# Kernel optimization log

Hardware: AMD Instinct MI355X
Metric: run time of the kernel (lower is better)

Reference implementation:

```python
import jax, jax.numpy as jnp
import numpy as np

IN_FEATURES = 8192
OUT_FEATURES = 8192
BATCH = 256


def setup_inputs() -> dict:
    key = jax.random.key(0)
    k_x, k_w, k_s, k_b = jax.random.split(key, 4)
    x = jax.random.normal(k_x, (BATCH, IN_FEATURES), dtype=jnp.float32)
    int8_weights = jax.random.randint(k_w, (OUT_FEATURES, IN_FEATURES), -128, 128, dtype=jnp.int8)
    int8_scales = jax.random.normal(k_s, (1,), dtype=jnp.float32)
    bias = jax.random.normal(k_b, (1, OUT_FEATURES), dtype=jnp.float32)
    return {"x": x, "int8_weights": int8_weights, "int8_scales": int8_scales, "bias": bias}


def reference(x, int8_weights, int8_scales, bias):
    # dequantize: symmetric per-tensor scale, then cast to activation dtype
    weights = int8_weights.astype(x.dtype) * int8_scales.astype(x.dtype)  # [out, in]
    # F.linear: x @ W^T
    out = jnp.einsum('bi,oi->bo', x, weights)
    out = out + bias
    return out
```

## Files before the change

### kernel.cpp

```cpp
#include <hip/hip_runtime.h>

#define M_DIM 256
#define N_DIM 8192
#define K_DIM 8192
#define BN 128
#define BK 32
#define KSPLIT 4
#define KLEN (K_DIM / KSPLIT)
#define NT (KLEN / BK)

typedef _Float16 half_t;
typedef __attribute__((ext_vector_type(8))) _Float16 half8;
typedef __attribute__((ext_vector_type(4))) float f32x4;
typedef __attribute__((ext_vector_type(4))) unsigned int u32x4;

__device__ __forceinline__ unsigned int pk2(float a, float b) {
  return __builtin_bit_cast(unsigned int, __builtin_amdgcn_cvt_pkrtz(a, b));
}

__global__ __launch_bounds__(512, 2) void qgemm(
    const float* __restrict__ x, const int* __restrict__ Wq,
    const float* __restrict__ scales, const float* __restrict__ bias,
    float* __restrict__ out) {
  __shared__ __align__(1024) char lds[49152];

  const int tid = threadIdx.x;
  const int bid = blockIdx.x;
  const int p = bid & 7;
  const int g = bid >> 3;
  const int ks = p >> 1;
  const int t = (g << 1) | (p & 1);
  const int col0 = t * BN;
  const int kbase = ks * KLEN;

  const int wid = tid >> 6, lane = tid & 63;
  const int wm = wid >> 1, wn = wid & 1;
  const int r16 = lane & 15, g4 = lane >> 4;

  const int xr = tid >> 1, xh2 = tid & 1;
  const int wr = tid >> 2, wc = tid & 3;

  const float* xp = x + (size_t)xr * K_DIM + kbase + xh2 * 16;
  const int* wp = Wq + (size_t)(col0 + wr) * K_DIM + kbase + wc * 8;

  const int sA = (xr >> 1) & 3;
  const int aw0 = xr * 64 + (((xh2 * 2 + 0) ^ sA) << 4);
  const int aw1 = xr * 64 + (((xh2 * 2 + 1) ^ sA) << 4);
  const int sB = (wr >> 1) & 3;
  const int bw0 = 16384 + wr * 64 + ((wc ^ sB) << 4);

  int aoff[4], boff[4];
#pragma unroll
  for (int mf = 0; mf < 4; ++mf) {
    int ra = wm * 64 + mf * 16 + r16;
    aoff[mf] = ra * 64 + ((g4 ^ ((ra >> 1) & 3)) << 4);
  }
#pragma unroll
  for (int nf = 0; nf < 4; ++nf) {
    int rb = wn * 64 + nf * 16 + r16;
    boff[nf] = 16384 + rb * 64 + ((g4 ^ ((rb >> 1) & 3)) << 4);
  }

  f32x4 acc[4][4];
#pragma unroll
  for (int i = 0; i < 4; ++i)
#pragma unroll
    for (int j = 0; j < 4; ++j) acc[i][j] = (f32x4){0.f, 0.f, 0.f, 0.f};

  float4 X0 = *(const float4*)(xp);
  float4 X1 = *(const float4*)(xp + 4);
  float4 X2 = *(const float4*)(xp + 8);
  float4 X3 = *(const float4*)(xp + 12);
  int4 Wa = *(const int4*)(wp);
  int4 Wb = *(const int4*)(wp + 4);

  for (int kt = 0; kt < NT; ++kt) {
    char* B0 = lds + (kt & 1) * 24576;

    u32x4 pa0, pa1, pb;
    pa0.x = pk2(X0.x, X0.y); pa0.y = pk2(X0.z, X0.w);
    pa0.z = pk2(X1.x, X1.y); pa0.w = pk2(X1.z, X1.w);
    pa1.x = pk2(X2.x, X2.y); pa1.y = pk2(X2.z, X2.w);
    pa1.z = pk2(X3.x, X3.y); pa1.w = pk2(X3.z, X3.w);
    pb.x = pk2((float)Wa.x, (float)Wa.y); pb.y = pk2((float)Wa.z, (float)Wa.w);
    pb.z = pk2((float)Wb.x, (float)Wb.y); pb.w = pk2((float)Wb.z, (float)Wb.w);
    *(u32x4*)(B0 + aw0) = pa0;
    *(u32x4*)(B0 + aw1) = pa1;
    *(u32x4*)(B0 + bw0) = pb;

    if (kt + 1 < NT) {
      xp += BK; wp += BK;
      X0 = *(const float4*)(xp);
      X1 = *(const float4*)(xp + 4);
      X2 = *(const float4*)(xp + 8);
      X3 = *(const float4*)(xp + 12);
      Wa = *(const int4*)(wp);
      Wb = *(const int4*)(wp + 4);
    }

    asm volatile("s_waitcnt lgkmcnt(0)" ::: "memory");
    __builtin_amdgcn_s_barrier();
    __builtin_amdgcn_sched_barrier(0);

    half8 af[4], bf[4];
#pragma unroll
    for (int mf = 0; mf < 4; ++mf) af[mf] = *(const half8*)(B0 + aoff[mf]);
#pragma unroll
    for (int nf = 0; nf < 4; ++nf) bf[nf] = *(const half8*)(B0 + boff[nf]);
#pragma unroll
    for (int mf = 0; mf < 4; ++mf)
#pragma unroll
      for (int nf = 0; nf < 4; ++nf)
        acc[mf][nf] = __builtin_amdgcn_mfma_f32_16x16x32_f16(
            af[mf], bf[nf], acc[mf][nf], 0, 0, 0);
  }

  const float scale = scales[0];
#pragma unroll
  for (int nf = 0; nf < 4; ++nf) {
    const int gcol = col0 + wn * 64 + nf * 16 + r16;
    const float bv = (ks == 0) ? bias[gcol] : 0.0f;
#pragma unroll
    for (int mf = 0; mf < 4; ++mf) {
      const int grow0 = wm * 64 + mf * 16 + g4 * 4;
#pragma unroll
      for (int j = 0; j < 4; ++j) {
        atomicAdd(out + (size_t)(grow0 + j) * N_DIM + gcol,
                  scale * acc[mf][nf][j] + bv);
      }
    }
  }
}

extern "C" void kernel_launch(void* const* d_in, const int* in_sizes, int n_in,
                              void* d_out, int out_size, void* d_ws, size_t ws_size,
                              hipStream_t stream) {
  const float* x = (const float*)d_in[0];
  const int* Wq = (const int*)d_in[1];
  const float* scales = (const float*)d_in[2];
  const float* bias = (const float*)d_in[3];
  float* out = (float*)d_out;

  hipMemsetAsync(d_out, 0, (size_t)M_DIM * N_DIM * sizeof(float), stream);
  qgemm<<<dim3(256), dim3(512), 0, stream>>>(x, Wq, scales, bias, out);
}
```

Baseline: 424.2 us.

## Pre-convert activations to fp16 tiles and stream them via direct global-to-LDS loads

```diff
diff --git a/kernel.cpp b/kernel.cpp
--- a/kernel.cpp
+++ b/kernel.cpp
@@ -8,6 +8,9 @@
 #define KSPLIT 4
 #define KLEN (K_DIM / KSPLIT)
 #define NT (KLEN / BK)
+#define ABYTES 16384
+#define BBYTES 8192
+#define BUFB (ABYTES + BBYTES)
 
 typedef _Float16 half_t;
 typedef __attribute__((ext_vector_type(8))) _Float16 half8;
@@ -17,12 +20,31 @@
 __device__ __forceinline__ unsigned int pk2(float a, float b) {
   return __builtin_bit_cast(unsigned int, __builtin_amdgcn_cvt_pkrtz(a, b));
 }
+__device__ __forceinline__ void gl16(const void* g, void* l) {
+  __builtin_amdgcn_global_load_lds(
+      (const __attribute__((address_space(1))) unsigned int*)g,
+      (__attribute__((address_space(3))) unsigned int*)l, 16, 0, 0);
+}
+
+__global__ __launch_bounds__(256) void convert_x(const float* __restrict__ x,
+                                                 half_t* __restrict__ xh) {
+  const int gid = blockIdx.x * 256 + threadIdx.x;
+  const int row = gid >> 10;
+  const int k0 = (gid & 1023) << 3;
+  float4 v0 = *(const float4*)(x + (size_t)row * K_DIM + k0);
+  float4 v1 = *(const float4*)(x + (size_t)row * K_DIM + k0 + 4);
+  half8 h;
+  h[0] = (half_t)v0.x; h[1] = (half_t)v0.y; h[2] = (half_t)v0.z; h[3] = (half_t)v0.w;
+  h[4] = (half_t)v1.x; h[5] = (half_t)v1.y; h[6] = (half_t)v1.z; h[7] = (half_t)v1.w;
+  const int kt = k0 >> 5, kk = k0 & 31;
+  *(half8*)(xh + (size_t)kt * 8192 + row * 32 + kk) = h;
+}
 
 __global__ __launch_bounds__(512, 2) void qgemm(
-    const float* __restrict__ x, const int* __restrict__ Wq,
+    const half_t* __restrict__ xh, const int* __restrict__ Wq,
     const float* __restrict__ scales, const float* __restrict__ bias,
     float* __restrict__ out) {
-  __shared__ __align__(1024) char lds[49152];
+  __shared__ __align__(1024) char lds[2 * BUFB];
 
   const int tid = threadIdx.x;
   const int bid = blockIdx.x;
@@ -31,35 +53,21 @@
   const int ks = p >> 1;
   const int t = (g << 1) | (p & 1);
   const int col0 = t * BN;
-  const int kbase = ks * KLEN;
 
   const int wid = tid >> 6, lane = tid & 63;
   const int wm = wid >> 1, wn = wid & 1;
   const int r16 = lane & 15, g4 = lane >> 4;
 
-  const int xr = tid >> 1, xh2 = tid & 1;
+  const half_t* abase = xh + (size_t)(ks * NT) * 8192;
   const int wr = tid >> 2, wc = tid & 3;
-
-  const float* xp = x + (size_t)xr * K_DIM + kbase + xh2 * 16;
-  const int* wp = Wq + (size_t)(col0 + wr) * K_DIM + kbase + wc * 8;
-
-  const int sA = (xr >> 1) & 3;
-  const int aw0 = xr * 64 + (((xh2 * 2 + 0) ^ sA) << 4);
-  const int aw1 = xr * 64 + (((xh2 * 2 + 1) ^ sA) << 4);
-  const int sB = (wr >> 1) & 3;
-  const int bw0 = 16384 + wr * 64 + ((wc ^ sB) << 4);
+  const int* wp0 = Wq + (size_t)(col0 + wr) * K_DIM + ks * KLEN + wc * 8;
+  const int wlds = ABYTES + wr * 64 + wc * 16;
 
   int aoff[4], boff[4];
 #pragma unroll
-  for (int mf = 0; mf < 4; ++mf) {
-    int ra = wm * 64 + mf * 16 + r16;
-    aoff[mf] = ra * 64 + ((g4 ^ ((ra >> 1) & 3)) << 4);
-  }
+  for (int mf = 0; mf < 4; ++mf) aoff[mf] = (wm * 64 + mf * 16 + r16) * 64 + g4 * 16;
 #pragma unroll
-  for (int nf = 0; nf < 4; ++nf) {
-    int rb = wn * 64 + nf * 16 + r16;
-    boff[nf] = 16384 + rb * 64 + ((g4 ^ ((rb >> 1) & 3)) << 4);
-  }
+  for (int nf = 0; nf < 4; ++nf) boff[nf] = ABYTES + (wn * 64 + nf * 16 + r16) * 64 + g4 * 16;
 
   f32x4 acc[4][4];
 #pragma unroll
@@ -67,52 +75,58 @@
 #pragma unroll
     for (int j = 0; j < 4; ++j) acc[i][j] = (f32x4){0.f, 0.f, 0.f, 0.f};
 
-  float4 X0 = *(const float4*)(xp);
-  float4 X1 = *(const float4*)(xp + 4);
-  float4 X2 = *(const float4*)(xp + 8);
-  float4 X3 = *(const float4*)(xp + 12);
-  int4 Wa = *(const int4*)(wp);
-  int4 Wb = *(const int4*)(wp + 4);
+  int4 Wa, Wb;
+  {
+    int4 w0a = *(const int4*)(wp0);
+    int4 w0b = *(const int4*)(wp0 + 4);
+    gl16(abase + tid * 8, lds + tid * 16);
+    gl16(abase + 4096 + tid * 8, lds + 8192 + tid * 16);
+    __builtin_amdgcn_sched_barrier(0);
+    u32x4 pb;
+    pb.x = pk2((float)w0a.x, (float)w0a.y); pb.y = pk2((float)w0a.z, (float)w0a.w);
+    pb.z = pk2((float)w0b.x, (float)w0b.y); pb.w = pk2((float)w0b.z, (float)w0b.w);
+    *(u32x4*)(lds + wlds) = pb;
+    Wa = *(const int4*)(wp0 + 32);
+    Wb = *(const int4*)(wp0 + 36);
+    __builtin_amdgcn_sched_barrier(0);
+    asm volatile("s_waitcnt vmcnt(2) lgkmcnt(0)" ::: "memory");
+    __builtin_amdgcn_s_barrier();
+  }
 
   for (int kt = 0; kt < NT; ++kt) {
-    char* B0 = lds + (kt & 1) * 24576;
+    char* Bc = lds + (kt & 1) * BUFB;
+    char* Bn = lds + ((kt & 1) ^ 1) * BUFB;
 
-    u32x4 pa0, pa1, pb;
-    pa0.x = pk2(X0.x, X0.y); pa0.y = pk2(X0.z, X0.w);
-    pa0.z = pk2(X1.x, X1.y); pa0.w = pk2(X1.z, X1.w);
-    pa1.x = pk2(X2.x, X2.y); pa1.y = pk2(X2.z, X2.w);
-    pa1.z = pk2(X3.x, X3.y); pa1.w = pk2(X3.z, X3.w);
+    u32x4 pb;
     pb.x = pk2((float)Wa.x, (float)Wa.y); pb.y = pk2((float)Wa.z, (float)Wa.w);
     pb.z = pk2((float)Wb.x, (float)Wb.y); pb.w = pk2((float)Wb.z, (float)Wb.w);
-    *(u32x4*)(B0 + aw0) = pa0;
-    *(u32x4*)(B0 + aw1) = pa1;
-    *(u32x4*)(B0 + bw0) = pb;
+    *(u32x4*)(Bn + wlds) = pb;
 
-    if (kt + 1 < NT) {
-      xp += BK; wp += BK;
-      X0 = *(const float4*)(xp);
-      X1 = *(const float4*)(xp + 4);
-      X2 = *(const float4*)(xp + 8);
-      X3 = *(const float4*)(xp + 12);
-      Wa = *(const int4*)(wp);
-      Wb = *(const int4*)(wp + 4);
-    }
+    const int an = (kt + 1 < NT) ? kt + 1 : NT - 1;
+    const half_t* asrc = abase + (size_t)an * 8192;
+    gl16(asrc + tid * 8, Bn + tid * 16);
+    gl16(asrc + 4096 + tid * 8, Bn + 8192 + tid * 16);
+    __builtin_amdgcn_sched_barrier(0);
 
-    asm volatile("s_waitcnt lgkmcnt(0)" ::: "memory");
-    __builtin_amdgcn_s_barrier();
-    __builtin_amdgcn_sched_barrier(0);
+    const int w2 = (kt + 2 < NT) ? kt + 2 : NT - 1;
+    Wa = *(const int4*)(wp0 + (size_t)w2 * 32);
+    Wb = *(const int4*)(wp0 + (size_t)w2 * 32 + 4);
 
     half8 af[4], bf[4];
 #pragma unroll
-    for (int mf = 0; mf < 4; ++mf) af[mf] = *(const half8*)(B0 + aoff[mf]);
+    for (int mf = 0; mf < 4; ++mf) af[mf] = *(const half8*)(Bc + aoff[mf]);
 #pragma unroll
-    for (int nf = 0; nf < 4; ++nf) bf[nf] = *(const half8*)(B0 + boff[nf]);
+    for (int nf = 0; nf < 4; ++nf) bf[nf] = *(const half8*)(Bc + boff[nf]);
 #pragma unroll
     for (int mf = 0; mf < 4; ++mf)
 #pragma unroll
       for (int nf = 0; nf < 4; ++nf)
         acc[mf][nf] = __builtin_amdgcn_mfma_f32_16x16x32_f16(
             af[mf], bf[nf], acc[mf][nf], 0, 0, 0);
+
+    __builtin_amdgcn_sched_barrier(0);
+    asm volatile("s_waitcnt vmcnt(2) lgkmcnt(0)" ::: "memory");
+    __builtin_amdgcn_s_barrier();
   }
 
   const float scale = scales[0];
@@ -140,7 +154,9 @@
   const float* scales = (const float*)d_in[2];
   const float* bias = (const float*)d_in[3];
   float* out = (float*)d_out;
+  half_t* xh = (half_t*)d_ws;
 
   hipMemsetAsync(d_out, 0, (size_t)M_DIM * N_DIM * sizeof(float), stream);
-  qgemm<<<dim3(256), dim3(512), 0, stream>>>(x, Wq, scales, bias, out);
+  convert_x<<<dim3(1024), dim3(256), 0, stream>>>(x, xh);
+  qgemm<<<dim3(256), dim3(512), 0, stream>>>(xh, Wq, scales, bias, out);
 }
```

Result: no change. 423.3 us (-0.2%).
